# Kernel tuning notes

Measured on AMD Instinct MI355X. Metric: run time of the kernel, lower is better.

Reference implementation:

```python
import jax, jax.numpy as jnp
import numpy as np

B, N, D, H = 32, 512, 1024, 16
HD = D // H          # head_dim = 64
SEG = 64             # seg_num (router set size, softmax axis)
FACTOR = N           # einsum forces factor == seq_len


def setup_inputs() -> dict:
    key = jax.random.key(0)
    ks = jax.random.split(key, 12)
    s = 0.02
    return {
        "query": jax.random.normal(ks[0], (B, N, D), jnp.float32),
        "key":   jax.random.normal(ks[1], (B, N, D), jnp.float32),
        "value": jax.random.normal(ks[2], (B, N, D), jnp.float32),
        "router": jax.random.normal(ks[3], (SEG, FACTOR, HD), jnp.float32),
        "Wq": jax.random.normal(ks[4], (D, D), jnp.float32) * s,
        "bq": jnp.zeros((D,), jnp.float32),
        "Wk": jax.random.normal(ks[5], (D, D), jnp.float32) * s,
        "bk": jnp.zeros((D,), jnp.float32),
        "Wv": jax.random.normal(ks[6], (D, D), jnp.float32) * s,
        "bv": jnp.zeros((D,), jnp.float32),
        "Wo": jax.random.normal(ks[7], (D, D), jnp.float32) * s,
        "bo": jnp.zeros((D,), jnp.float32),
    }


def reference(query, key, value, router, Wq, bq, Wk, bk, Wv, bv, Wo, bo):
    b = query.shape[0]
    q = query @ Wq + bq                      # (B, N, D)
    k = key @ Wk + bk                        # computed but unused (faithful to source)
    v = value @ Wv + bv                      # computed but unused (faithful to source)
    # (B, N, H, HD) -> (B, H, N, HD)
    qh = q.reshape(b, -1, H, HD).transpose(0, 2, 1, 3)
    # torch: einsum('bnhd,bfhd->bnhf', q_bHnd, router_bSFd); shared 'h' = seq/factor
    # scores: (B, H, N, SEG); softmax over router/segment axis
    scores = jnp.einsum('bhnd,snd->bhns', qh, router)
    attn = jax.nn.softmax(scores, axis=-1)   # dropout = identity (eval mode)
    # combine: (B, H, N, HD)
    received = jnp.einsum('bhns,snd->bhnd', attn, router)
    received = received.transpose(0, 2, 1, 3).reshape(b, -1, D)
    output = received @ Wo + bo              # (B, N, D)
    return output, attn
```

## Files before the change

kernel.cpp:

```cpp
#include <hip/hip_runtime.h>

#define DEV __device__ __forceinline__

typedef __attribute__((ext_vector_type(8))) short bf16x8;
typedef __attribute__((ext_vector_type(4))) float f32x4;

constexpr int Bc  = 32;
constexpr int Nc  = 512;
constexpr int Dc  = 1024;
constexpr int Hc  = 16;
constexpr int HDc = 64;
constexpr int SEGc= 64;
constexpr int Mrows = Bc * Nc;

DEV unsigned short bf16r(float x) {
  union { float f; unsigned int u; } c; c.f = x;
  unsigned int r = (c.u + 0x7fffu + ((c.u >> 16) & 1u)) >> 16;
  return (unsigned short)r;
}

DEV void async_ld16(const void* g, void* l) {
  __builtin_amdgcn_global_load_lds(
      (const __attribute__((address_space(1))) void*)g,
      (__attribute__((address_space(3))) void*)l,
      16, 0, 0);
}

__global__ void transpose_bf16(const float* __restrict__ src,
                               unsigned short* __restrict__ dst) {
  __shared__ float tile[32][33];
  int bx = blockIdx.x & 31, by = blockIdx.x >> 5;
  int tx = threadIdx.x & 31, ty = threadIdx.x >> 5;
  for (int i = 0; i < 4; ++i) {
    int r = ty + i * 8;
    tile[r][tx] = src[(size_t)(by * 32 + r) * 1024 + bx * 32 + tx];
  }
  __syncthreads();
  for (int i = 0; i < 4; ++i) {
    int r = ty + i * 8;
    dst[(size_t)(bx * 32 + r) * 1024 + by * 32 + tx] = bf16r(tile[tx][r]);
  }
}

__global__ void wq_tile(const float* __restrict__ src,
                        unsigned short* __restrict__ dst) {
  __shared__ float tile[32][33];
  int bx = blockIdx.x & 31, by = blockIdx.x >> 5;
  int tx = threadIdx.x & 31, ty = threadIdx.x >> 5;
  for (int i = 0; i < 4; ++i) {
    int r = ty + i * 8;
    tile[r][tx] = src[(size_t)(by * 32 + r) * 1024 + bx * 32 + tx];
  }
  __syncthreads();
  if (ty < 4) {
    int oct = ty;
    unsigned short tmp[8];
#pragma unroll
    for (int e = 0; e < 8; ++e) tmp[e] = bf16r(tile[oct * 8 + e][tx]);
    ushort4 u0, u1;
    u0.x = tmp[0]; u0.y = tmp[1]; u0.z = tmp[2]; u0.w = tmp[3];
    u1.x = tmp[4]; u1.y = tmp[5]; u1.z = tmp[6]; u1.w = tmp[7];
    size_t idx = (size_t)by * 32768 + (size_t)oct * 8192 + (size_t)(bx * 32 + tx) * 8;
    *(ushort4*)(dst + idx) = u0;
    *(ushort4*)(dst + idx + 4) = u1;
  }
}

__global__ void cvt_router2(const float* __restrict__ src,
                            unsigned short* __restrict__ Rg,
                            unsigned short* __restrict__ RTg) {
  int nn = blockIdx.x;
  int t  = threadIdx.x;
  int s  = t >> 2, dq = (t & 3) * 16;
  const float* p = src + ((size_t)s * 512 + nn) * 64 + dq;
  float v[16];
#pragma unroll
  for (int i = 0; i < 16; i += 4) {
    float4 f = *(const float4*)(p + i);
    v[i] = f.x; v[i+1] = f.y; v[i+2] = f.z; v[i+3] = f.w;
  }
  unsigned short bv[16];
#pragma unroll
  for (int i = 0; i < 16; ++i) bv[i] = bf16r(v[i]);
  unsigned short* rb = Rg + (size_t)nn * 4096 + s * 64;
#pragma unroll
  for (int o2 = 0; o2 < 2; ++o2) {
    int oct  = (dq >> 3) + o2;
    int phys = oct ^ (s & 7);
    ushort4 a, b2;
    a.x  = bv[o2*8+0]; a.y  = bv[o2*8+1]; a.z  = bv[o2*8+2]; a.w  = bv[o2*8+3];
    b2.x = bv[o2*8+4]; b2.y = bv[o2*8+5]; b2.z = bv[o2*8+6]; b2.w = bv[o2*8+7];
    *(ushort4*)(rb + phys * 8)     = a;
    *(ushort4*)(rb + phys * 8 + 4) = b2;
  }
  unsigned short* tb = RTg + (size_t)nn * 4096;
#pragma unroll
  for (int i = 0; i < 16; ++i) {
    int d = dq + i;
    tb[d * 64 + (((s >> 3) ^ (d & 7)) * 8) + (s & 7)] = bv[i];
  }
}

template <bool OUT_F32>
__global__ __launch_bounds__(256)
void gemm_bt(const unsigned short* __restrict__ A,
             const unsigned short* __restrict__ BT,
             const float* __restrict__ bias,
             void* __restrict__ Cout) {
  constexpr int K = 1024, Nn = 1024, BM = 128, BK = 32;
  __shared__ unsigned short As[BM * BK];
  __shared__ unsigned short Bs[BM * BK];
  const int tid = threadIdx.x, lane = tid & 63, wave = tid >> 6;
  const int tm = blockIdx.x >> 3, tn = blockIdx.x & 7;
  const int wm = (wave >> 1) * 64, wn = (wave & 1) * 64;
  const int la = lane & 15, quad = lane >> 4, lb8 = quad * 8;

  f32x4 acc[4][4] = {};

  const int srow = tid >> 2;
  const int scol = (tid & 3) * 8;
  const unsigned short* Ag = A  + (size_t)(tm * BM + srow) * K + scol;
  const unsigned short* Bg = BT + (size_t)(tn * BM + srow) * K + scol;
  unsigned short* ldsA = As + wave * 512;
  unsigned short* ldsB = Bs + wave * 512;

  for (int k0 = 0; k0 < K; k0 += BK) {
    __syncthreads();
    async_ld16(Ag + k0,          ldsA);
    async_ld16(Ag + 64 * K + k0, ldsA + 2048);
    async_ld16(Bg + k0,          ldsB);
    async_ld16(Bg + 64 * K + k0, ldsB + 2048);
    __syncthreads();

    bf16x8 af[4], bfr[4];
#pragma unroll
    for (int i = 0; i < 4; ++i)
      af[i] = *(const bf16x8*)(As + (wm + i * 16 + la) * BK + lb8);
#pragma unroll
    for (int j = 0; j < 4; ++j)
      bfr[j] = *(const bf16x8*)(Bs + (wn + j * 16 + la) * BK + lb8);
#pragma unroll
    for (int i = 0; i < 4; ++i)
#pragma unroll
      for (int j = 0; j < 4; ++j)
        acc[i][j] = __builtin_amdgcn_mfma_f32_16x16x32_bf16(af[i], bfr[j],
                                                            acc[i][j], 0, 0, 0);
  }

  const int colbase = tn * BM + wn;
  float bv[4];
#pragma unroll
  for (int j = 0; j < 4; ++j) bv[j] = bias[colbase + j * 16 + la];

  float* eps = (wave < 2) ? ((float*)As) + wave * 1024
                          : ((float*)Bs) + (wave - 2) * 1024;
  const int rowbase = tm * BM + wm;

#pragma unroll
  for (int i = 0; i < 4; ++i) {
    __syncthreads();
#pragma unroll
    for (int j = 0; j < 4; ++j)
#pragma unroll
      for (int r = 0; r < 4; ++r)
        eps[(quad * 4 + r) * 64 + j * 16 + la] = acc[i][j][r] + bv[j];
    __syncthreads();
#pragma unroll
    for (int s = 0; s < 4; ++s) {
      int idx = s * 64 + lane;
      int row = idx >> 4, c4 = idx & 15;
      float4 v = *(const float4*)(eps + row * 64 + c4 * 4);
      size_t goff = (size_t)(rowbase + i * 16 + row) * Nn + colbase + c4 * 4;
      if (OUT_F32) {
        *(float4*)((float*)Cout + goff) = v;
      } else {
        ushort4 u;
        u.x = bf16r(v.x); u.y = bf16r(v.y); u.z = bf16r(v.z); u.w = bf16r(v.w);
        *(ushort4*)((unsigned short*)Cout + goff) = u;
      }
    }
  }
}

__global__ __launch_bounds__(512, 2)
void fused_qmid(const float* __restrict__ query,
                const unsigned short* __restrict__ wqt,
                const float* __restrict__ bq,
                const unsigned short* __restrict__ Rg,
                const unsigned short* __restrict__ RTg,
                float* __restrict__ attn_out,
                unsigned short* __restrict__ recv_out) {
  __shared__ __align__(16) unsigned short lds[69632];
  const int tid = threadIdx.x, lane = tid & 63, w = tid >> 6;
  const int la = lane & 15, quad = lane >> 4;
  const int n0 = blockIdx.x * 2;

  f32x4 acc[4][8] = {};

  const int arow = tid >> 3;
  const int ag   = tid & 7;
  const int a_b  = arow & 31, a_nl = arow >> 5;
  const float* aq = query + ((size_t)(a_b * 512 + n0 + a_nl)) * 1024 + ag * 4;
  const int a_lidx = (ag >> 1) * 512 + arow * 8 + (ag & 1) * 4;
  const int bslot  = w * 512 + lane * 8;

  {
    float4 qv = *(const float4*)(aq);
#pragma unroll
    for (int p = 0; p < 8; ++p)
      async_ld16(wqt + p * 4096 + bslot, lds + p * 4096 + w * 512);
    ushort4 u;
    u.x = bf16r(qv.x); u.y = bf16r(qv.y); u.z = bf16r(qv.z); u.w = bf16r(qv.w);
    *(ushort4*)(lds + 65536 + a_lidx) = u;
  }
  __syncthreads();

#pragma unroll 1
  for (int kb = 0; kb < 32; ++kb) {
    const int cur = kb & 1;
    unsigned short* Bc_ = lds + cur * 32768;
    unsigned short* Ac_ = lds + 65536 + cur * 2048;
    unsigned short* Bn_ = lds + (cur ^ 1) * 32768;
    unsigned short* An_ = lds + 65536 + (cur ^ 1) * 2048;

    float4 qv;
    if (kb < 31) {
      qv = *(const float4*)(aq + (kb + 1) * 32);
#pragma unroll
      for (int p = 0; p < 8; ++p)
        async_ld16(wqt + (size_t)(kb + 1) * 32768 + p * 4096 + bslot,
                   Bn_ + p * 4096 + w * 512);
    }

    bf16x8 af[4], bfr[8];
#pragma unroll
    for (int rt = 0; rt < 4; ++rt)
      af[rt] = *(const bf16x8*)(Ac_ + quad * 512 + (rt * 16 + la) * 8);
#pragma unroll
    for (int j = 0; j < 8; ++j)
      bfr[j] = *(const bf16x8*)(Bc_ + quad * 8192 + ((w * 8 + j) * 16 + la) * 8);
#pragma unroll
    for (int rt = 0; rt < 4; ++rt)
#pragma unroll
      for (int j = 0; j < 8; ++j)
        acc[rt][j] = __builtin_amdgcn_mfma_f32_16x16x32_bf16(af[rt], bfr[j],
                                                             acc[rt][j], 0, 0, 0);
    if (kb < 31) {
      ushort4 u;
      u.x = bf16r(qv.x); u.y = bf16r(qv.y); u.z = bf16r(qv.z); u.w = bf16r(qv.w);
      *(ushort4*)(An_ + a_lidx) = u;
    }
    __syncthreads();
  }

  float bv[8];
#pragma unroll
  for (int j = 0; j < 8; ++j) bv[j] = bq[(w * 8 + j) * 16 + la];
#pragma unroll
  for (int rt = 0; rt < 4; ++rt)
#pragma unroll
    for (int j = 0; j < 8; ++j)
#pragma unroll
      for (int r = 0; r < 4; ++r) acc[rt][j][r] += bv[j];

#pragma unroll
  for (int q2 = 0; q2 < 4; ++q2) {
    const unsigned short* srcb = (q2 < 2) ? (Rg  + (size_t)(n0 + q2)     * 4096)
                                          : (RTg + (size_t)(n0 + q2 - 2) * 4096);
    async_ld16(srcb + bslot, lds + 49152 + q2 * 4096 + w * 512);
  }
  __syncthreads();

  unsigned short* Qs = lds + w * 6144;
  unsigned short* AT = lds + w * 6144 + 3072;
  const unsigned short* Rsb  = lds + 49152;
  const unsigned short* RTsb = lds + 57344;

#pragma unroll
  for (int nl = 0; nl < 2; ++nl) {
#pragma unroll
    for (int hh = 0; hh < 2; ++hh) {
      const int h  = w * 2 + hh;
      const int nn = n0 + nl;

#pragma unroll
      for (int rt2 = 0; rt2 < 2; ++rt2)
#pragma unroll
        for (int j4 = 0; j4 < 4; ++j4)
#pragma unroll
          for (int r = 0; r < 4; ++r) {
            int b_ = rt2 * 16 + quad * 4 + r;
            int d_ = j4 * 16 + la;
            Qs[b_ * 72 + d_] = bf16r(acc[nl * 2 + rt2][hh * 4 + j4][r]);
          }

      bf16x8 qf[2][2], rf[4][2];
#pragma unroll
      for (int bt = 0; bt < 2; ++bt)
#pragma unroll
        for (int kc = 0; kc < 2; ++kc)
          qf[bt][kc] = *(const bf16x8*)(Qs + (bt * 16 + la) * 72 + (kc * 4 + quad) * 8);
      const unsigned short* Rn = Rsb + nl * 4096;
#pragma unroll
      for (int st = 0; st < 4; ++st)
#pragma unroll
        for (int kc = 0; kc < 2; ++kc) {
          int s_ = st * 16 + la;
          rf[st][kc] = *(const bf16x8*)(Rn + s_ * 64 + ((kc * 4 + quad) ^ (s_ & 7)) * 8);
        }

      f32x4 sacc[2][4] = {};
#pragma unroll
      for (int bt = 0; bt < 2; ++bt)
#pragma unroll
        for (int st = 0; st < 4; ++st) {
          sacc[bt][st] = __builtin_amdgcn_mfma_f32_16x16x32_bf16(rf[st][0], qf[bt][0], sacc[bt][st], 0, 0, 0);
          sacc[bt][st] = __builtin_amdgcn_mfma_f32_16x16x32_bf16(rf[st][1], qf[bt][1], sacc[bt][st], 0, 0, 0);
        }

#pragma unroll
      for (int bt = 0; bt < 2; ++bt) {
        float mx = sacc[bt][0][0];
#pragma unroll
        for (int st = 0; st < 4; ++st)
#pragma unroll
          for (int r = 0; r < 4; ++r) mx = fmaxf(mx, sacc[bt][st][r]);
        mx = fmaxf(mx, __shfl_xor(mx, 16));
        mx = fmaxf(mx, __shfl_xor(mx, 32));
        float sum = 0.f;
#pragma unroll
        for (int st = 0; st < 4; ++st)
#pragma unroll
          for (int r = 0; r < 4; ++r) {
            float e = __expf(sacc[bt][st][r] - mx);
            sacc[bt][st][r] = e; sum += e;
          }
        sum += __shfl_xor(sum, 16);
        sum += __shfl_xor(sum, 32);
        float inv = 1.0f / sum;
#pragma unroll
        for (int st = 0; st < 4; ++st) {
          sacc[bt][st][0] *= inv; sacc[bt][st][1] *= inv;
          sacc[bt][st][2] *= inv; sacc[bt][st][3] *= inv;
        }
        const int b_ = bt * 16 + la;
        float* ao = attn_out + ((size_t)(b_ * 16 + h) * 512 + nn) * 64 + quad * 4;
#pragma unroll
        for (int st = 0; st < 4; ++st) {
          *(float4*)(ao + st * 16) = *(float4*)(&sacc[bt][st]);
          ushort4 u;
          u.x = bf16r(sacc[bt][st][0]); u.y = bf16r(sacc[bt][st][1]);
          u.z = bf16r(sacc[bt][st][2]); u.w = bf16r(sacc[bt][st][3]);
          *(ushort4*)(AT + b_ * 72 + st * 16 + quad * 4) = u;
        }
      }

      bf16x8 atf[2][2], rtf2[4][2];
#pragma unroll
      for (int bt = 0; bt < 2; ++bt)
#pragma unroll
        for (int kc = 0; kc < 2; ++kc)
          atf[bt][kc] = *(const bf16x8*)(AT + (bt * 16 + la) * 72 + (kc * 4 + quad) * 8);
      const unsigned short* RTn = RTsb + nl * 4096;
#pragma unroll
      for (int dt = 0; dt < 4; ++dt)
#pragma unroll
        for (int kc = 0; kc < 2; ++kc) {
          int d_ = dt * 16 + la;
          rtf2[dt][kc] = *(const bf16x8*)(RTn + d_ * 64 + ((kc * 4 + quad) ^ (d_ & 7)) * 8);
        }
      f32x4 racc[2][4] = {};
#pragma unroll
      for (int bt = 0; bt < 2; ++bt)
#pragma unroll
        for (int dt = 0; dt < 4; ++dt) {
          racc[bt][dt] = __builtin_amdgcn_mfma_f32_16x16x32_bf16(rtf2[dt][0], atf[bt][0], racc[bt][dt], 0, 0, 0);
          racc[bt][dt] = __builtin_amdgcn_mfma_f32_16x16x32_bf16(rtf2[dt][1], atf[bt][1], racc[bt][dt], 0, 0, 0);
        }

#pragma unroll
      for (int bt = 0; bt < 2; ++bt) {
        const int b_ = bt * 16 + la;
        unsigned short* ro = recv_out + ((size_t)(b_ * 512 + nn)) * 1024
                           + h * 64 + quad * 4;
#pragma unroll
        for (int dt = 0; dt < 4; ++dt) {
          ushort4 u;
          u.x = bf16r(racc[bt][dt][0]); u.y = bf16r(racc[bt][dt][1]);
          u.z = bf16r(racc[bt][dt][2]); u.w = bf16r(racc[bt][dt][3]);
          *(ushort4*)(ro + dt * 16) = u;
        }
      }
    }
  }
}

extern "C" void kernel_launch(void* const* d_in, const int* in_sizes, int n_in,
                              void* d_out, int out_size, void* d_ws, size_t ws_size,
                              hipStream_t stream) {
  const float* query  = (const float*)d_in[0];
  const float* router = (const float*)d_in[3];
  const float* Wq     = (const float*)d_in[4];
  const float* bq     = (const float*)d_in[5];
  const float* Wo     = (const float*)d_in[10];
  const float* bo     = (const float*)d_in[11];

  float* out      = (float*)d_out;
  float* attn_out = out + (size_t)Bc * Nc * Dc;

  char* ws = (char*)d_ws;
  unsigned short* recv_b = (unsigned short*)(ws);
  unsigned short* WqTile = (unsigned short*)(ws + 33554432u);
  unsigned short* WoT    = (unsigned short*)(ws + 35651584u);
  unsigned short* Rg     = (unsigned short*)(ws + 37748736u);
  unsigned short* RTg    = (unsigned short*)(ws + 41943040u);

  wq_tile       <<<1024, 256, 0, stream>>>(Wq, WqTile);
  transpose_bf16<<<1024, 256, 0, stream>>>(Wo, WoT);
  cvt_router2   <<<512,  256, 0, stream>>>(router, Rg, RTg);
  fused_qmid    <<<256,  512, 0, stream>>>(query, WqTile, bq, Rg, RTg,
                                           attn_out, recv_b);
  gemm_bt<true> <<<(Mrows / 128) * 8, 256, 0, stream>>>(recv_b, WoT, bo, out);
}
```

Baseline: 376.0 us.

## Split fused Q-projection kernel across column halves and merge prep kernels

The fused Q-projection/router kernel now launches twice as many blocks, each computing half of the output columns (8 heads), which halves its accumulator registers and LDS footprint. The Wq tile layout and the A-tile layout in LDS gain an XOR swizzle to cut bank conflicts, and the router tiles are prefetched during the last K iteration instead of after the loop. The three weight and router conversion kernels are merged into one launch. The trade-off is that each query tile is now loaded and converted twice, once per column half.

```diff
diff --git a/kernel.cpp b/kernel.cpp
--- a/kernel.cpp
+++ b/kernel.cpp
@@ -26,78 +26,77 @@
       16, 0, 0);
 }
 
-__global__ void transpose_bf16(const float* __restrict__ src,
-                               unsigned short* __restrict__ dst) {
-  __shared__ float tile[32][33];
-  int bx = blockIdx.x & 31, by = blockIdx.x >> 5;
-  int tx = threadIdx.x & 31, ty = threadIdx.x >> 5;
-  for (int i = 0; i < 4; ++i) {
-    int r = ty + i * 8;
-    tile[r][tx] = src[(size_t)(by * 32 + r) * 1024 + bx * 32 + tx];
-  }
-  __syncthreads();
-  for (int i = 0; i < 4; ++i) {
-    int r = ty + i * 8;
-    dst[(size_t)(bx * 32 + r) * 1024 + by * 32 + tx] = bf16r(tile[tx][r]);
-  }
-}
-
-__global__ void wq_tile(const float* __restrict__ src,
-                        unsigned short* __restrict__ dst) {
-  __shared__ float tile[32][33];
-  int bx = blockIdx.x & 31, by = blockIdx.x >> 5;
-  int tx = threadIdx.x & 31, ty = threadIdx.x >> 5;
-  for (int i = 0; i < 4; ++i) {
-    int r = ty + i * 8;
-    tile[r][tx] = src[(size_t)(by * 32 + r) * 1024 + bx * 32 + tx];
-  }
-  __syncthreads();
-  if (ty < 4) {
-    int oct = ty;
-    unsigned short tmp[8];
-#pragma unroll
-    for (int e = 0; e < 8; ++e) tmp[e] = bf16r(tile[oct * 8 + e][tx]);
-    ushort4 u0, u1;
-    u0.x = tmp[0]; u0.y = tmp[1]; u0.z = tmp[2]; u0.w = tmp[3];
-    u1.x = tmp[4]; u1.y = tmp[5]; u1.z = tmp[6]; u1.w = tmp[7];
-    size_t idx = (size_t)by * 32768 + (size_t)oct * 8192 + (size_t)(bx * 32 + tx) * 8;
-    *(ushort4*)(dst + idx) = u0;
-    *(ushort4*)(dst + idx + 4) = u1;
-  }
-}
-
-__global__ void cvt_router2(const float* __restrict__ src,
-                            unsigned short* __restrict__ Rg,
-                            unsigned short* __restrict__ RTg) {
-  int nn = blockIdx.x;
-  int t  = threadIdx.x;
-  int s  = t >> 2, dq = (t & 3) * 16;
-  const float* p = src + ((size_t)s * 512 + nn) * 64 + dq;
-  float v[16];
-#pragma unroll
-  for (int i = 0; i < 16; i += 4) {
-    float4 f = *(const float4*)(p + i);
-    v[i] = f.x; v[i+1] = f.y; v[i+2] = f.z; v[i+3] = f.w;
-  }
-  unsigned short bv[16];
-#pragma unroll
-  for (int i = 0; i < 16; ++i) bv[i] = bf16r(v[i]);
-  unsigned short* rb = Rg + (size_t)nn * 4096 + s * 64;
-#pragma unroll
-  for (int o2 = 0; o2 < 2; ++o2) {
-    int oct  = (dq >> 3) + o2;
-    int phys = oct ^ (s & 7);
-    ushort4 a, b2;
-    a.x  = bv[o2*8+0]; a.y  = bv[o2*8+1]; a.z  = bv[o2*8+2]; a.w  = bv[o2*8+3];
-    b2.x = bv[o2*8+4]; b2.y = bv[o2*8+5]; b2.z = bv[o2*8+6]; b2.w = bv[o2*8+7];
-    *(ushort4*)(rb + phys * 8)     = a;
-    *(ushort4*)(rb + phys * 8 + 4) = b2;
-  }
-  unsigned short* tb = RTg + (size_t)nn * 4096;
-#pragma unroll
-  for (int i = 0; i < 16; ++i) {
-    int d = dq + i;
-    tb[d * 64 + (((s >> 3) ^ (d & 7)) * 8) + (s & 7)] = bv[i];
+__global__ __launch_bounds__(256)
+void prep(const float* __restrict__ Wq, const float* __restrict__ Wo,
+          const float* __restrict__ router,
+          unsigned short* __restrict__ wqt, unsigned short* __restrict__ WoT,
+          unsigned short* __restrict__ Rg, unsigned short* __restrict__ RTg) {
+  const int bid = blockIdx.x;
+  if (bid < 2048) {
+    __shared__ float tile[32][33];
+    const bool isWq = bid < 1024;
+    const int b2 = isWq ? bid : bid - 1024;
+    const float* src = isWq ? Wq : Wo;
+    const int bx = b2 & 31, by = b2 >> 5;
+    const int tx = threadIdx.x & 31, ty = threadIdx.x >> 5;
+    for (int i = 0; i < 4; ++i) {
+      int r = ty + i * 8;
+      tile[r][tx] = src[(size_t)(by * 32 + r) * 1024 + bx * 32 + tx];
+    }
+    __syncthreads();
+    if (isWq) {
+      if (ty < 4) {
+        const int oct = ty;
+        const int c = bx * 32 + tx, cbb = c >> 9, cl = c & 511;
+        const int cphys = cl ^ (oct << 1);
+        unsigned short tmp[8];
+#pragma unroll
+        for (int e = 0; e < 8; ++e) tmp[e] = bf16r(tile[oct * 8 + e][tx]);
+        ushort4 u0, u1;
+        u0.x = tmp[0]; u0.y = tmp[1]; u0.z = tmp[2]; u0.w = tmp[3];
+        u1.x = tmp[4]; u1.y = tmp[5]; u1.z = tmp[6]; u1.w = tmp[7];
+        size_t idx = (size_t)cbb * 524288 + (size_t)by * 16384
+                   + (size_t)oct * 4096 + (size_t)cphys * 8;
+        *(ushort4*)(wqt + idx)     = u0;
+        *(ushort4*)(wqt + idx + 4) = u1;
+      }
+    } else {
+      for (int i = 0; i < 4; ++i) {
+        int r = ty + i * 8;
+        WoT[(size_t)(bx * 32 + r) * 1024 + by * 32 + tx] = bf16r(tile[tx][r]);
+      }
+    }
+  } else {
+    const int nn = bid - 2048;
+    const int t  = threadIdx.x;
+    const int s  = t >> 2, dq = (t & 3) * 16;
+    const float* p = router + ((size_t)s * 512 + nn) * 64 + dq;
+    float v[16];
+#pragma unroll
+    for (int i = 0; i < 16; i += 4) {
+      float4 f = *(const float4*)(p + i);
+      v[i] = f.x; v[i+1] = f.y; v[i+2] = f.z; v[i+3] = f.w;
+    }
+    unsigned short bvv[16];
+#pragma unroll
+    for (int i = 0; i < 16; ++i) bvv[i] = bf16r(v[i]);
+    unsigned short* rb = Rg + (size_t)nn * 4096 + s * 64;
+#pragma unroll
+    for (int o2 = 0; o2 < 2; ++o2) {
+      int oct  = (dq >> 3) + o2;
+      int phys = oct ^ (s & 7);
+      ushort4 a, b2v;
+      a.x   = bvv[o2*8+0]; a.y   = bvv[o2*8+1]; a.z   = bvv[o2*8+2]; a.w   = bvv[o2*8+3];
+      b2v.x = bvv[o2*8+4]; b2v.y = bvv[o2*8+5]; b2v.z = bvv[o2*8+6]; b2v.w = bvv[o2*8+7];
+      *(ushort4*)(rb + phys * 8)     = a;
+      *(ushort4*)(rb + phys * 8 + 4) = b2v;
+    }
+    unsigned short* tb = RTg + (size_t)nn * 4096;
+#pragma unroll
+    for (int i = 0; i < 16; ++i) {
+      int d = dq + i;
+      tb[d * 64 + (((s >> 3) ^ (d & 7)) * 8) + (s & 7)] = bvv[i];
+    }
   }
 }
 
@@ -182,7 +181,7 @@
   }
 }
 
-__global__ __launch_bounds__(512, 2)
+__global__ __launch_bounds__(512)
 void fused_qmid(const float* __restrict__ query,
                 const unsigned short* __restrict__ wqt,
                 const float* __restrict__ bq,
@@ -190,59 +189,71 @@
                 const unsigned short* __restrict__ RTg,
                 float* __restrict__ attn_out,
                 unsigned short* __restrict__ recv_out) {
-  __shared__ __align__(16) unsigned short lds[69632];
+  __shared__ __align__(16) unsigned short lds[36864];
   const int tid = threadIdx.x, lane = tid & 63, w = tid >> 6;
   const int la = lane & 15, quad = lane >> 4;
-  const int n0 = blockIdx.x * 2;
-
-  f32x4 acc[4][8] = {};
+  const int n0 = (blockIdx.x >> 1) * 2, cbh = blockIdx.x & 1;
+
+  f32x4 acc[4][4] = {};
 
   const int arow = tid >> 3;
   const int ag   = tid & 7;
   const int a_b  = arow & 31, a_nl = arow >> 5;
   const float* aq = query + ((size_t)(a_b * 512 + n0 + a_nl)) * 1024 + ag * 4;
-  const int a_lidx = (ag >> 1) * 512 + arow * 8 + (ag & 1) * 4;
+  const int a_oct  = ag >> 1;
+  const int a_lidx = a_oct * 512 + (arow ^ (a_oct << 1)) * 8 + (ag & 1) * 4;
   const int bslot  = w * 512 + lane * 8;
+  const unsigned short* wqb = wqt + (size_t)cbh * 524288;
 
   {
     float4 qv = *(const float4*)(aq);
 #pragma unroll
-    for (int p = 0; p < 8; ++p)
-      async_ld16(wqt + p * 4096 + bslot, lds + p * 4096 + w * 512);
+    for (int p = 0; p < 4; ++p)
+      async_ld16(wqb + p * 4096 + bslot, lds + p * 4096 + w * 512);
     ushort4 u;
     u.x = bf16r(qv.x); u.y = bf16r(qv.y); u.z = bf16r(qv.z); u.w = bf16r(qv.w);
-    *(ushort4*)(lds + 65536 + a_lidx) = u;
+    *(ushort4*)(lds + 32768 + a_lidx) = u;
   }
   __syncthreads();
 
 #pragma unroll 1
   for (int kb = 0; kb < 32; ++kb) {
     const int cur = kb & 1;
-    unsigned short* Bc_ = lds + cur * 32768;
-    unsigned short* Ac_ = lds + 65536 + cur * 2048;
-    unsigned short* Bn_ = lds + (cur ^ 1) * 32768;
-    unsigned short* An_ = lds + 65536 + (cur ^ 1) * 2048;
+    unsigned short* Bc_ = lds + cur * 16384;
+    unsigned short* Ac_ = lds + 32768 + cur * 2048;
+    unsigned short* Bn_ = lds + (cur ^ 1) * 16384;
+    unsigned short* An_ = lds + 32768 + (cur ^ 1) * 2048;
 
     float4 qv;
     if (kb < 31) {
       qv = *(const float4*)(aq + (kb + 1) * 32);
 #pragma unroll
-      for (int p = 0; p < 8; ++p)
-        async_ld16(wqt + (size_t)(kb + 1) * 32768 + p * 4096 + bslot,
+      for (int p = 0; p < 4; ++p)
+        async_ld16(wqb + (size_t)(kb + 1) * 16384 + p * 4096 + bslot,
                    Bn_ + p * 4096 + w * 512);
-    }
-
-    bf16x8 af[4], bfr[8];
+    } else {
+#pragma unroll
+      for (int q2 = 0; q2 < 4; ++q2) {
+        const unsigned short* srcb = (q2 < 2)
+            ? (Rg  + (size_t)(n0 + q2)     * 4096)
+            : (RTg + (size_t)(n0 + q2 - 2) * 4096);
+        async_ld16(srcb + bslot, lds + q2 * 4096 + w * 512);
+      }
+    }
+
+    bf16x8 af[4], bfr[4];
 #pragma unroll
     for (int rt = 0; rt < 4; ++rt)
-      af[rt] = *(const bf16x8*)(Ac_ + quad * 512 + (rt * 16 + la) * 8);
-#pragma unroll
-    for (int j = 0; j < 8; ++j)
-      bfr[j] = *(const bf16x8*)(Bc_ + quad * 8192 + ((w * 8 + j) * 16 + la) * 8);
+      af[rt] = *(const bf16x8*)(Ac_ + quad * 512
+                                + ((rt * 16 + la) ^ (quad << 1)) * 8);
+#pragma unroll
+    for (int j = 0; j < 4; ++j)
+      bfr[j] = *(const bf16x8*)(Bc_ + quad * 4096
+                                + (((w * 4 + j) * 16 + la) ^ (quad << 1)) * 8);
 #pragma unroll
     for (int rt = 0; rt < 4; ++rt)
 #pragma unroll
-      for (int j = 0; j < 8; ++j)
+      for (int j = 0; j < 4; ++j)
         acc[rt][j] = __builtin_amdgcn_mfma_f32_16x16x32_bf16(af[rt], bfr[j],
                                                              acc[rt][j], 0, 0, 0);
     if (kb < 31) {
@@ -253,143 +264,132 @@
     __syncthreads();
   }
 
-  float bv[8];
-#pragma unroll
-  for (int j = 0; j < 8; ++j) bv[j] = bq[(w * 8 + j) * 16 + la];
+  float bv[4];
+#pragma unroll
+  for (int j = 0; j < 4; ++j) bv[j] = bq[cbh * 512 + (w * 4 + j) * 16 + la];
 #pragma unroll
   for (int rt = 0; rt < 4; ++rt)
 #pragma unroll
-    for (int j = 0; j < 8; ++j)
+    for (int j = 0; j < 4; ++j)
 #pragma unroll
       for (int r = 0; r < 4; ++r) acc[rt][j][r] += bv[j];
 
-#pragma unroll
-  for (int q2 = 0; q2 < 4; ++q2) {
-    const unsigned short* srcb = (q2 < 2) ? (Rg  + (size_t)(n0 + q2)     * 4096)
-                                          : (RTg + (size_t)(n0 + q2 - 2) * 4096);
-    async_ld16(srcb + bslot, lds + 49152 + q2 * 4096 + w * 512);
-  }
-  __syncthreads();
-
-  unsigned short* Qs = lds + w * 6144;
-  unsigned short* AT = lds + w * 6144 + 3072;
-  const unsigned short* Rsb  = lds + 49152;
-  const unsigned short* RTsb = lds + 57344;
+  const int h = cbh * 8 + w;
+  unsigned short* QA = lds + 16384 + w * 2304;
 
 #pragma unroll
   for (int nl = 0; nl < 2; ++nl) {
-#pragma unroll
-    for (int hh = 0; hh < 2; ++hh) {
-      const int h  = w * 2 + hh;
-      const int nn = n0 + nl;
-
-#pragma unroll
-      for (int rt2 = 0; rt2 < 2; ++rt2)
-#pragma unroll
-        for (int j4 = 0; j4 < 4; ++j4)
-#pragma unroll
-          for (int r = 0; r < 4; ++r) {
-            int b_ = rt2 * 16 + quad * 4 + r;
-            int d_ = j4 * 16 + la;
-            Qs[b_ * 72 + d_] = bf16r(acc[nl * 2 + rt2][hh * 4 + j4][r]);
-          }
-
-      bf16x8 qf[2][2], rf[4][2];
-#pragma unroll
-      for (int bt = 0; bt < 2; ++bt)
-#pragma unroll
-        for (int kc = 0; kc < 2; ++kc)
-          qf[bt][kc] = *(const bf16x8*)(Qs + (bt * 16 + la) * 72 + (kc * 4 + quad) * 8);
-      const unsigned short* Rn = Rsb + nl * 4096;
+    const int nn = n0 + nl;
+
+#pragma unroll
+    for (int rt2 = 0; rt2 < 2; ++rt2)
+#pragma unroll
+      for (int j4 = 0; j4 < 4; ++j4)
+#pragma unroll
+        for (int r = 0; r < 4; ++r)
+          QA[(rt2 * 16 + quad * 4 + r) * 72 + j4 * 16 + la]
+              = bf16r(acc[nl * 2 + rt2][j4][r]);
+
+    bf16x8 qf[2][2], rf[4][2];
+#pragma unroll
+    for (int bt = 0; bt < 2; ++bt)
+#pragma unroll
+      for (int kc = 0; kc < 2; ++kc)
+        qf[bt][kc] = *(const bf16x8*)(QA + (bt * 16 + la) * 72
+                                      + (kc * 4 + quad) * 8);
+    const unsigned short* Rn = lds + nl * 4096;
+#pragma unroll
+    for (int st = 0; st < 4; ++st)
+#pragma unroll
+      for (int kc = 0; kc < 2; ++kc) {
+        int s_ = st * 16 + la;
+        rf[st][kc] = *(const bf16x8*)(Rn + s_ * 64
+                                      + ((kc * 4 + quad) ^ (s_ & 7)) * 8);
+      }
+
+    f32x4 sacc[2][4] = {};
+#pragma unroll
+    for (int bt = 0; bt < 2; ++bt)
+#pragma unroll
+      for (int st = 0; st < 4; ++st) {
+        sacc[bt][st] = __builtin_amdgcn_mfma_f32_16x16x32_bf16(rf[st][0], qf[bt][0], sacc[bt][st], 0, 0, 0);
+        sacc[bt][st] = __builtin_amdgcn_mfma_f32_16x16x32_bf16(rf[st][1], qf[bt][1], sacc[bt][st], 0, 0, 0);
+      }
+
+#pragma unroll
+    for (int bt = 0; bt < 2; ++bt) {
+      float mx = sacc[bt][0][0];
 #pragma unroll
       for (int st = 0; st < 4; ++st)
 #pragma unroll
-        for (int kc = 0; kc < 2; ++kc) {
-          int s_ = st * 16 + la;
-          rf[st][kc] = *(const bf16x8*)(Rn + s_ * 64 + ((kc * 4 + quad) ^ (s_ & 7)) * 8);
+        for (int r = 0; r < 4; ++r) mx = fmaxf(mx, sacc[bt][st][r]);
+      mx = fmaxf(mx, __shfl_xor(mx, 16));
+      mx = fmaxf(mx, __shfl_xor(mx, 32));
+      float sum = 0.f;
+#pragma unroll
+      for (int st = 0; st < 4; ++st)
+#pragma unroll
+        for (int r = 0; r < 4; ++r) {
+          float e = __expf(sacc[bt][st][r] - mx);
+          sacc[bt][st][r] = e; sum += e;
         }
-
-      f32x4 sacc[2][4] = {};
-#pragma unroll
-      for (int bt = 0; bt < 2; ++bt)
-#pragma unroll
-        for (int st = 0; st < 4; ++st) {
-          sacc[bt][st] = __builtin_amdgcn_mfma_f32_16x16x32_bf16(rf[st][0], qf[bt][0], sacc[bt][st], 0, 0, 0);
-          sacc[bt][st] = __builtin_amdgcn_mfma_f32_16x16x32_bf16(rf[st][1], qf[bt][1], sacc[bt][st], 0, 0, 0);
-        }
-
-#pragma unroll
-      for (int bt = 0; bt < 2; ++bt) {
-        float mx = sacc[bt][0][0];
-#pragma unroll
-        for (int st = 0; st < 4; ++st)
-#pragma unroll
-          for (int r = 0; r < 4; ++r) mx = fmaxf(mx, sacc[bt][st][r]);
-        mx = fmaxf(mx, __shfl_xor(mx, 16));
-        mx = fmaxf(mx, __shfl_xor(mx, 32));
-        float sum = 0.f;
-#pragma unroll
-        for (int st = 0; st < 4; ++st)
-#pragma unroll
-          for (int r = 0; r < 4; ++r) {
-            float e = __expf(sacc[bt][st][r] - mx);
-            sacc[bt][st][r] = e; sum += e;
-          }
-        sum += __shfl_xor(sum, 16);
-        sum += __shfl_xor(sum, 32);
-        float inv = 1.0f / sum;
-#pragma unroll
-        for (int st = 0; st < 4; ++st) {
-          sacc[bt][st][0] *= inv; sacc[bt][st][1] *= inv;
-          sacc[bt][st][2] *= inv; sacc[bt][st][3] *= inv;
-        }
-        const int b_ = bt * 16 + la;
-        float* ao = attn_out + ((size_t)(b_ * 16 + h) * 512 + nn) * 64 + quad * 4;
-#pragma unroll
-        for (int st = 0; st < 4; ++st) {
-          *(float4*)(ao + st * 16) = *(float4*)(&sacc[bt][st]);
-          ushort4 u;
-          u.x = bf16r(sacc[bt][st][0]); u.y = bf16r(sacc[bt][st][1]);
-          u.z = bf16r(sacc[bt][st][2]); u.w = bf16r(sacc[bt][st][3]);
-          *(ushort4*)(AT + b_ * 72 + st * 16 + quad * 4) = u;
-        }
-      }
-
-      bf16x8 atf[2][2], rtf2[4][2];
-#pragma unroll
-      for (int bt = 0; bt < 2; ++bt)
-#pragma unroll
-        for (int kc = 0; kc < 2; ++kc)
-          atf[bt][kc] = *(const bf16x8*)(AT + (bt * 16 + la) * 72 + (kc * 4 + quad) * 8);
-      const unsigned short* RTn = RTsb + nl * 4096;
-#pragma unroll
-      for (int dt = 0; dt < 4; ++dt)
-#pragma unroll
-        for (int kc = 0; kc < 2; ++kc) {
-          int d_ = dt * 16 + la;
-          rtf2[dt][kc] = *(const bf16x8*)(RTn + d_ * 64 + ((kc * 4 + quad) ^ (d_ & 7)) * 8);
-        }
-      f32x4 racc[2][4] = {};
-#pragma unroll
-      for (int bt = 0; bt < 2; ++bt)
-#pragma unroll
-        for (int dt = 0; dt < 4; ++dt) {
-          racc[bt][dt] = __builtin_amdgcn_mfma_f32_16x16x32_bf16(rtf2[dt][0], atf[bt][0], racc[bt][dt], 0, 0, 0);
-          racc[bt][dt] = __builtin_amdgcn_mfma_f32_16x16x32_bf16(rtf2[dt][1], atf[bt][1], racc[bt][dt], 0, 0, 0);
-        }
-
-#pragma unroll
-      for (int bt = 0; bt < 2; ++bt) {
-        const int b_ = bt * 16 + la;
-        unsigned short* ro = recv_out + ((size_t)(b_ * 512 + nn)) * 1024
-                           + h * 64 + quad * 4;
-#pragma unroll
-        for (int dt = 0; dt < 4; ++dt) {
-          ushort4 u;
-          u.x = bf16r(racc[bt][dt][0]); u.y = bf16r(racc[bt][dt][1]);
-          u.z = bf16r(racc[bt][dt][2]); u.w = bf16r(racc[bt][dt][3]);
-          *(ushort4*)(ro + dt * 16) = u;
-        }
+      sum += __shfl_xor(sum, 16);
+      sum += __shfl_xor(sum, 32);
+      float inv = 1.0f / sum;
+#pragma unroll
+      for (int st = 0; st < 4; ++st) {
+        sacc[bt][st][0] *= inv; sacc[bt][st][1] *= inv;
+        sacc[bt][st][2] *= inv; sacc[bt][st][3] *= inv;
+      }
+      const int b_ = bt * 16 + la;
+      float* ao = attn_out + ((size_t)(b_ * 16 + h) * 512 + nn) * 64 + quad * 4;
+#pragma unroll
+      for (int st = 0; st < 4; ++st) {
+        *(float4*)(ao + st * 16) = *(float4*)(&sacc[bt][st]);
+        ushort4 u;
+        u.x = bf16r(sacc[bt][st][0]); u.y = bf16r(sacc[bt][st][1]);
+        u.z = bf16r(sacc[bt][st][2]); u.w = bf16r(sacc[bt][st][3]);
+        *(ushort4*)(QA + b_ * 72 + st * 16 + quad * 4) = u;
+      }
+    }
+
+    __asm__ volatile("s_waitcnt lgkmcnt(0)" ::: "memory");
+    bf16x8 atf[2][2], rtf2[4][2];
+#pragma unroll
+    for (int bt = 0; bt < 2; ++bt)
+#pragma unroll
+      for (int kc = 0; kc < 2; ++kc)
+        atf[bt][kc] = *(const bf16x8*)(QA + (bt * 16 + la) * 72
+                                       + (kc * 4 + quad) * 8);
+    const unsigned short* RTn = lds + 8192 + nl * 4096;
+#pragma unroll
+    for (int dt = 0; dt < 4; ++dt)
+#pragma unroll
+      for (int kc = 0; kc < 2; ++kc) {
+        int d_ = dt * 16 + la;
+        rtf2[dt][kc] = *(const bf16x8*)(RTn + d_ * 64
+                                        + ((kc * 4 + quad) ^ (d_ & 7)) * 8);
+      }
+    f32x4 racc[2][4] = {};
+#pragma unroll
+    for (int bt = 0; bt < 2; ++bt)
+#pragma unroll
+      for (int dt = 0; dt < 4; ++dt) {
+        racc[bt][dt] = __builtin_amdgcn_mfma_f32_16x16x32_bf16(rtf2[dt][0], atf[bt][0], racc[bt][dt], 0, 0, 0);
+        racc[bt][dt] = __builtin_amdgcn_mfma_f32_16x16x32_bf16(rtf2[dt][1], atf[bt][1], racc[bt][dt], 0, 0, 0);
+      }
+
+#pragma unroll
+    for (int bt = 0; bt < 2; ++bt) {
+      const int b_ = bt * 16 + la;
+      unsigned short* ro = recv_out + ((size_t)(b_ * 512 + nn)) * 1024
+                         + h * 64 + quad * 4;
+#pragma unroll
+      for (int dt = 0; dt < 4; ++dt) {
+        ushort4 u;
+        u.x = bf16r(racc[bt][dt][0]); u.y = bf16r(racc[bt][dt][1]);
+        u.z = bf16r(racc[bt][dt][2]); u.w = bf16r(racc[bt][dt][3]);
+        *(ushort4*)(ro + dt * 16) = u;
       }
     }
   }
@@ -415,10 +415,8 @@
   unsigned short* Rg     = (unsigned short*)(ws + 37748736u);
   unsigned short* RTg    = (unsigned short*)(ws + 41943040u);
 
-  wq_tile       <<<1024, 256, 0, stream>>>(Wq, WqTile);
-  transpose_bf16<<<1024, 256, 0, stream>>>(Wo, WoT);
-  cvt_router2   <<<512,  256, 0, stream>>>(router, Rg, RTg);
-  fused_qmid    <<<256,  512, 0, stream>>>(query, WqTile, bq, Rg, RTg,
-                                           attn_out, recv_b);
-  gemm_bt<true> <<<(Mrows / 128) * 8, 256, 0, stream>>>(recv_b, WoT, bo, out);
-}
+  prep         <<<2560, 256, 0, stream>>>(Wq, Wo, router, WqTile, WoT, Rg, RTg);
+  fused_qmid   <<<512,  512, 0, stream>>>(query, WqTile, bq, Rg, RTg,
+                                          attn_out, recv_b);
+  gemm_bt<true><<<(Mrows / 128) * 8, 256, 0, stream>>>(recv_b, WoT, bo, out);
+}
```

After: 378.9 us. No clear change (+0.8%).
